# Performance work log

Hardware: AMD Instinct MI355X
Metric: run time of the kernel (lower is better)

Reference implementation:

```python
import jax, jax.numpy as jnp
import numpy as np

# Quantization constants from __init__ (num_bits=8, in_min=-1, in_max=1)
IN_MIN, IN_MAX = -1.0, 1.0
QMAX = 2 ** 8 - 1  # 255
IN_SCALE = (IN_MAX - IN_MIN) / QMAX
IN_ZP = round(-IN_MIN / (IN_SCALE + 1e-12))  # 128
W_SCALE = 0.01
B_SCALE = 0.0001

TOKENS, D_IN, D_OUT = 8192, 4096, 4096


def setup_inputs() -> dict:
    key = jax.random.key(0)
    k1, k2, k3 = jax.random.split(key, 3)
    x_float = jax.random.normal(k1, (TOKENS, D_IN), dtype=jnp.float32)
    # w_q / b_q are pre-quantized integer values stored as float (as in layer_params)
    w_q = jnp.round(jnp.clip(jax.random.normal(k2, (D_OUT, D_IN), dtype=jnp.float32) * 40.0, -128.0, 127.0))
    b_q = jnp.round(jnp.clip(jax.random.normal(k3, (D_OUT,), dtype=jnp.float32) * 40.0, -128.0, 127.0))
    return {"x_float": x_float, "w_q": w_q, "b_q": b_q}


def reference(x_float, w_q, b_q):
    # Fake-quant the activations: round-half-to-even (matches torch.round), clamp to uint8 range
    x_q = jnp.clip(jnp.round(x_float / IN_SCALE + IN_ZP), 0.0, 255.0)
    x_shifted = x_q - IN_ZP
    # Integer-valued GEMM computed in float: [T, D_in] x [D_out, D_in]^T -> [T, D_out]
    acc_int = jnp.einsum("ti,oi->to", x_shifted, w_q)
    out = acc_int * (IN_SCALE * W_SCALE) + b_q * B_SCALE
    return out
```

## Files before the change

### kernel.cpp

```cpp
#include <hip/hip_runtime.h>
#include <hip/hip_bf16.h>
#include <stdint.h>


#define TOKENS 8192
#define DIN    4096
#define DOUT   4096

typedef int v4i __attribute__((ext_vector_type(4)));

#define IN_SCALE_F ((float)(2.0/255.0))
#define SF  ((float)((2.0/255.0)*0.01))
#define BSF (1e-4f)

typedef const __attribute__((address_space(1))) void* gas_ptr;
typedef __attribute__((address_space(3))) void* las_ptr;
#define GLL16(g, s) __builtin_amdgcn_global_load_lds((gas_ptr)(g), (las_ptr)(s), 16, 0, 0)

__device__ __forceinline__ int quant1(float x) {
    float v = rintf(x / IN_SCALE_F + 127.0f);
    v = fminf(fmaxf(v, 0.0f), 255.0f);
    return (int)v - 128;
}

__global__ void quant_x(const float* __restrict__ x, signed char* __restrict__ xq) {
    const int n4 = TOKENS * DIN / 4;
    const float4* x4 = (const float4*)x;
    int* o4 = (int*)xq;
    int i = blockIdx.x * blockDim.x + threadIdx.x;
    int stride = gridDim.x * blockDim.x;
    for (; i < n4; i += stride) {
        float4 v = x4[i];
        int q0 = quant1(v.x), q1 = quant1(v.y), q2 = quant1(v.z), q3 = quant1(v.w);
        o4[i] = (q0 & 255) | ((q1 & 255) << 8) | ((q2 & 255) << 16) | ((q3 & 255) << 24);
    }
}

__global__ void prep_w(const float* __restrict__ w, const float* __restrict__ bq,
                       signed char* __restrict__ wq, float* __restrict__ beta) {
    int row = blockIdx.x, t = threadIdx.x;
    const float4* wrow = (const float4*)(w + (size_t)row * DIN);
    int* wqrow = (int*)(wq + (size_t)row * DIN);
    int s = 0;
#pragma unroll
    for (int it = 0; it < 4; ++it) {
        int idx = it * 256 + t;
        float4 v = wrow[idx];
        int a0 = (int)v.x, a1 = (int)v.y, a2 = (int)v.z, a3 = (int)v.w;
        s += a0 + a1 + a2 + a3;
        wqrow[idx] = (a0 & 255) | ((a1 & 255) << 8) | ((a2 & 255) << 16) | ((a3 & 255) << 24);
    }
#pragma unroll
    for (int off = 32; off > 0; off >>= 1) s += __shfl_down(s, off);
    __shared__ int red[4];
    if ((t & 63) == 0) red[t >> 6] = s;
    __syncthreads();
    if (t == 0) beta[row] = (float)(red[0] + red[1] + red[2] + red[3]) * SF + bq[row] * BSF;
}

#define BM 256
#define BN 256
#define BKI 64
#define NT (DIN / BKI)
#define BUFB 32768

__global__ __launch_bounds__(512, 1) void gemm_i8(const signed char* __restrict__ A,
                                                  const signed char* __restrict__ B,
                                                  const float* __restrict__ beta,
                                                  float* __restrict__ out) {
    __shared__ signed char lds[4 * BUFB];
    const int tid = threadIdx.x;
    const int w = tid >> 6, l = tid & 63;
    const int wm = w >> 2, wn = w & 3;

    const int bid = blockIdx.x;
    const int swz = (bid & 7) * 64 + (bid >> 3);
    const int bm = swz >> 4;
    const int bn = swz & 15;
    const int m0 = bm * BM, n0 = bn * BN;

    const int row0 = tid >> 2, slot0 = tid & 3;
    const size_t src0 = (size_t)row0 * DIN + (size_t)((slot0 ^ (row0 & 3)) * 16);
    const size_t src1 = src0 + (size_t)128 * DIN;
    const unsigned l0 = (unsigned)tid * 16;
    const unsigned l1 = 8192 + (unsigned)tid * 16;
    const signed char* Abase = A + (size_t)m0 * DIN;
    const signed char* Bbase = B + (size_t)n0 * DIN;

#define STAGE(tb, kk) do {                                        \
        const signed char* _a = Abase + (kk);                     \
        const signed char* _b = Bbase + (kk);                     \
        signed char* _l = lds + (tb) * BUFB;                      \
        GLL16(_a + src0, _l + l0);                                \
        GLL16(_a + src1, _l + l1);                                \
        GLL16(_b + src0, _l + 16384 + l0);                        \
        GLL16(_b + src1, _l + 16384 + l1);                        \
    } while (0)

    const int xslot = (l >> 4) ^ (l & 3);
    const unsigned abase = (unsigned)(wm * 8192 + (l & 15) * 64 + xslot * 16);
    const unsigned bbase = (unsigned)(16384 + wn * 4096 + (l & 15) * 64 + xslot * 16);

    v4i acc[8][4];
#pragma unroll
    for (int mf = 0; mf < 8; ++mf)
#pragma unroll
        for (int nf = 0; nf < 4; ++nf) acc[mf][nf] = (v4i)0;

    STAGE(0, 0);
    STAGE(1, BKI);
    STAGE(2, 2 * BKI);

#pragma unroll 4
    for (int t = 0; t < NT; ++t) {
        const int ts = t + 3;
        STAGE(ts & 3, (ts & (NT - 1)) * BKI);

        asm volatile("s_waitcnt vmcnt(12)" ::: "memory");
        __builtin_amdgcn_s_barrier();
        __builtin_amdgcn_sched_barrier(0);

        const signed char* Lc = lds + (t & 3) * BUFB;
        v4i af[8], bf[4];
#pragma unroll
        for (int mf = 0; mf < 8; ++mf) af[mf] = *(const v4i*)(Lc + abase + mf * 1024);
#pragma unroll
        for (int nf = 0; nf < 4; ++nf) bf[nf] = *(const v4i*)(Lc + bbase + nf * 1024);

        __builtin_amdgcn_s_setprio(1);
#pragma unroll
        for (int mf = 0; mf < 8; ++mf)
#pragma unroll
            for (int nf = 0; nf < 4; ++nf)
                acc[mf][nf] = __builtin_amdgcn_mfma_i32_16x16x64_i8(af[mf], bf[nf], acc[mf][nf], 0, 0, 0);
        __builtin_amdgcn_s_setprio(0);

        __builtin_amdgcn_s_barrier();
        __builtin_amdgcn_sched_barrier(0);
    }
#undef STAGE

    const int col0 = n0 + wn * 64 + (l & 15);
    const int row0o = m0 + wm * 128 + (l >> 4) * 4;
#pragma unroll
    for (int nf = 0; nf < 4; ++nf) {
        const float bb = beta[col0 + nf * 16];
#pragma unroll
        for (int mf = 0; mf < 8; ++mf) {
#pragma unroll
            for (int r = 0; r < 4; ++r) {
                out[(size_t)(row0o + mf * 16 + r) * DOUT + (col0 + nf * 16)] =
                    (float)acc[mf][nf][r] * SF + bb;
            }
        }
    }
}

__global__ __launch_bounds__(256) void gemm_fb(const float* __restrict__ x,
                                               const float* __restrict__ wgt,
                                               const float* __restrict__ bq,
                                               float* __restrict__ out) {
    __shared__ float As[64][33];
    __shared__ float Bs[64][33];
    const int t = threadIdx.x;
    const int bn = blockIdx.x & 63;
    const int bm = blockIdx.x >> 6;
    const int m0 = bm * 64, n0 = bn * 64;
    const int ty = t >> 4, tx = t & 15;

    float acc[4][4] = {{0.f}};

    for (int k0 = 0; k0 < DIN; k0 += 32) {
#pragma unroll
        for (int i = 0; i < 8; ++i) {
            int li = t * 8 + i;
            int r = li >> 5, c = li & 31;
            float v = x[(size_t)(m0 + r) * DIN + k0 + c];
            float q = fminf(fmaxf(rintf(v / IN_SCALE_F + 127.0f), 0.0f), 255.0f) - 127.0f;
            As[r][c] = q;
            Bs[r][c] = wgt[(size_t)(n0 + r) * DIN + k0 + c];
        }
        __syncthreads();
#pragma unroll 8
        for (int k = 0; k < 32; ++k) {
            float a0 = As[ty * 4 + 0][k], a1 = As[ty * 4 + 1][k];
            float a2 = As[ty * 4 + 2][k], a3 = As[ty * 4 + 3][k];
            float b0 = Bs[tx * 4 + 0][k], b1 = Bs[tx * 4 + 1][k];
            float b2 = Bs[tx * 4 + 2][k], b3 = Bs[tx * 4 + 3][k];
            acc[0][0] += a0 * b0; acc[0][1] += a0 * b1; acc[0][2] += a0 * b2; acc[0][3] += a0 * b3;
            acc[1][0] += a1 * b0; acc[1][1] += a1 * b1; acc[1][2] += a1 * b2; acc[1][3] += a1 * b3;
            acc[2][0] += a2 * b0; acc[2][1] += a2 * b1; acc[2][2] += a2 * b2; acc[2][3] += a2 * b3;
            acc[3][0] += a3 * b0; acc[3][1] += a3 * b1; acc[3][2] += a3 * b2; acc[3][3] += a3 * b3;
        }
        __syncthreads();
    }

#pragma unroll
    for (int i = 0; i < 4; ++i)
#pragma unroll
        for (int j = 0; j < 4; ++j) {
            int col = n0 + tx * 4 + j;
            out[(size_t)(m0 + ty * 4 + i) * DOUT + col] = acc[i][j] * SF + bq[col] * BSF;
        }
}

extern "C" void kernel_launch(void* const* d_in, const int* in_sizes, int n_in,
                              void* d_out, int out_size, void* d_ws, size_t ws_size,
                              hipStream_t stream) {
    const float* x = (const float*)d_in[0];
    const float* wgt = (const float*)d_in[1];
    const float* bq = (const float*)d_in[2];
    float* out = (float*)d_out;

    const size_t need = (size_t)TOKENS * DIN + (size_t)DOUT * DIN + (size_t)DOUT * sizeof(float);

    if (d_ws != nullptr && ws_size >= need) {
        signed char* xq = (signed char*)d_ws;
        signed char* wq = xq + (size_t)TOKENS * DIN;
        float* beta = (float*)(wq + (size_t)DOUT * DIN);

        quant_x<<<2048, 256, 0, stream>>>(x, xq);
        prep_w<<<DOUT, 256, 0, stream>>>(wgt, bq, wq, beta);
        gemm_i8<<<(TOKENS / BM) * (DOUT / BN), 512, 0, stream>>>(xq, wq, beta, out);
    } else {
        gemm_fb<<<(TOKENS / 64) * (DOUT / 64), 256, 0, stream>>>(x, wgt, bq, out);
    }
}
```

Before: 408.3 us.

## Interleave LDS fragment reads with MFMA phases and use one barrier per k-step

The int8 GEMM main loop is restructured. The wait-and-barrier for the next tile now sits at the end of each iteration, so there is one barrier per k-step instead of two. A-fragment LDS reads are split into four phases that interleave with groups of MFMAs, which lets LDS latency overlap with matrix work. The LDS XOR swizzle now keys on (row>>1)&3 to change the bank-conflict pattern, and launch_bounds asks for 2 blocks per CU. That request tightens the register budget and may cause spills, while the 128KB of LDS per block may still allow only one resident block.

```diff
diff --git a/kernel.cpp b/kernel.cpp
--- a/kernel.cpp
+++ b/kernel.cpp
@@ -64,7 +64,7 @@
 #define NT (DIN / BKI)
 #define BUFB 32768
 
-__global__ __launch_bounds__(512, 1) void gemm_i8(const signed char* __restrict__ A,
+__global__ __launch_bounds__(512, 2) void gemm_i8(const signed char* __restrict__ A,
                                                   const signed char* __restrict__ B,
                                                   const float* __restrict__ beta,
                                                   float* __restrict__ out) {
@@ -79,8 +79,8 @@
     const int bn = swz & 15;
     const int m0 = bm * BM, n0 = bn * BN;
 
-    const int row0 = tid >> 2, slot0 = tid & 3;
-    const size_t src0 = (size_t)row0 * DIN + (size_t)((slot0 ^ (row0 & 3)) * 16);
+    const int row0 = tid >> 2;
+    const size_t src0 = (size_t)row0 * DIN + (size_t)(((tid & 3) ^ ((tid >> 3) & 3)) * 16);
     const size_t src1 = src0 + (size_t)128 * DIN;
     const unsigned l0 = (unsigned)tid * 16;
     const unsigned l1 = 8192 + (unsigned)tid * 16;
@@ -97,7 +97,7 @@
         GLL16(_b + src1, _l + 16384 + l1);                        \
     } while (0)
 
-    const int xslot = (l >> 4) ^ (l & 3);
+    const int xslot = (l >> 4) ^ ((l >> 1) & 3);
     const unsigned abase = (unsigned)(wm * 8192 + (l & 15) * 64 + xslot * 16);
     const unsigned bbase = (unsigned)(16384 + wn * 4096 + (l & 15) * 64 + xslot * 16);
 
@@ -110,34 +110,42 @@
     STAGE(0, 0);
     STAGE(1, BKI);
     STAGE(2, 2 * BKI);
+    asm volatile("s_waitcnt vmcnt(8)" ::: "memory");
+    __builtin_amdgcn_s_barrier();
+
+#define RD(off) (*(const v4i*)(Lc + (off)))
+#define PHASE(g, afA, afB)                                                             \
+    __builtin_amdgcn_sched_barrier(0);                                                 \
+    __builtin_amdgcn_s_setprio(1);                                                     \
+    _Pragma("unroll")                                                                  \
+    for (int nf = 0; nf < 4; ++nf) {                                                   \
+        acc[2*(g)][nf]   = __builtin_amdgcn_mfma_i32_16x16x64_i8(afA, bf[nf], acc[2*(g)][nf],   0, 0, 0); \
+        acc[2*(g)+1][nf] = __builtin_amdgcn_mfma_i32_16x16x64_i8(afB, bf[nf], acc[2*(g)+1][nf], 0, 0, 0); \
+    }                                                                                  \
+    __builtin_amdgcn_s_setprio(0);
 
 #pragma unroll 4
     for (int t = 0; t < NT; ++t) {
         const int ts = t + 3;
         STAGE(ts & 3, (ts & (NT - 1)) * BKI);
 
-        asm volatile("s_waitcnt vmcnt(12)" ::: "memory");
+        const signed char* Lc = lds + (t & 3) * BUFB;
+        v4i af0 = RD(abase), af1 = RD(abase + 1024);
+        v4i bf[4] = { RD(bbase), RD(bbase + 1024), RD(bbase + 2048), RD(bbase + 3072) };
+        PHASE(0, af0, af1)
+        v4i af2 = RD(abase + 2048), af3 = RD(abase + 3072);
+        PHASE(1, af2, af3)
+        v4i af4 = RD(abase + 4096), af5 = RD(abase + 5120);
+        PHASE(2, af4, af5)
+        v4i af6 = RD(abase + 6144), af7 = RD(abase + 7168);
+        PHASE(3, af6, af7)
+
+        asm volatile("s_waitcnt vmcnt(8)" ::: "memory");
         __builtin_amdgcn_s_barrier();
         __builtin_amdgcn_sched_barrier(0);
-
-        const signed char* Lc = lds + (t & 3) * BUFB;
-        v4i af[8], bf[4];
-#pragma unroll
-        for (int mf = 0; mf < 8; ++mf) af[mf] = *(const v4i*)(Lc + abase + mf * 1024);
-#pragma unroll
-        for (int nf = 0; nf < 4; ++nf) bf[nf] = *(const v4i*)(Lc + bbase + nf * 1024);
-
-        __builtin_amdgcn_s_setprio(1);
-#pragma unroll
-        for (int mf = 0; mf < 8; ++mf)
-#pragma unroll
-            for (int nf = 0; nf < 4; ++nf)
-                acc[mf][nf] = __builtin_amdgcn_mfma_i32_16x16x64_i8(af[mf], bf[nf], acc[mf][nf], 0, 0, 0);
-        __builtin_amdgcn_s_setprio(0);
-
-        __builtin_amdgcn_s_barrier();
-        __builtin_amdgcn_sched_barrier(0);
-    }
+    }
+#undef PHASE
+#undef RD
 #undef STAGE
 
     const int col0 = n0 + wn * 64 + (l & 15);
```

Measured after the change: 403.6 us. No clear change (-1.1%).
